# Kernel optimization log

Hardware: AMD Instinct MI355X
Metric: run time of the kernel (lower is better)

## Reference

```python
import jax, jax.numpy as jnp
import numpy as np

B, N, FN, FE, OUT = 64, 128, 64, 16, 128
S, VOCAB, EMB, LH = 1033, 1033, 50, 8
MOMO, SIDE, T = 200, 963, 3
LN_EPS, BN_EPS = 1e-12, 1e-5


def setup_inputs():
    key = jax.random.key(0)
    ks = iter(jax.random.split(key, 64))
    def nrm(shape, scale=0.05):
        return jax.random.normal(next(ks), shape, dtype=jnp.float32) * scale
    inp = {}
    inp['adjacency_1'] = (jax.random.uniform(next(ks), (B, N, N)) < 0.1).astype(jnp.float32)
    inp['nodes_1'] = nrm((B, N, FN), 1.0)
    inp['edges_1'] = nrm((B, N, N, FE), 1.0)
    inp['adjacency_2'] = (jax.random.uniform(next(ks), (B, N, N)) < 0.1).astype(jnp.float32)
    inp['nodes_2'] = nrm((B, N, FN), 1.0)
    inp['edges_2'] = nrm((B, N, N, FE), 1.0)
    inp['d1_momo_fts'] = nrm((B, MOMO), 1.0)
    inp['d2_momo_fts'] = nrm((B, MOMO), 1.0)
    inp['d1_protein_fts'] = jax.random.randint(next(ks), (B, S), 0, VOCAB)
    inp['d2_protein_fts'] = jax.random.randint(next(ks), (B, S), 0, VOCAB)
    inp['side_effect'] = nrm((B, SIDE), 1.0)
    inp['word_emb'] = nrm((VOCAB, EMB))
    inp['pos_emb'] = nrm((VOCAB, EMB))
    inp['ln_gamma'] = jnp.ones((EMB,), jnp.float32)
    inp['ln_beta'] = jnp.zeros((EMB,), jnp.float32)
    inp['W_ih'] = nrm((4 * LH, EMB))
    inp['W_hh'] = nrm((4 * LH, LH))
    inp['b_ih'] = jnp.zeros((4 * LH,), jnp.float32)
    inp['b_hh'] = jnp.zeros((4 * LH,), jnp.float32)
    inp['dec_W1'] = nrm((LH * S, 256))
    inp['dec_b1'] = jnp.zeros((256,), jnp.float32)
    inp['bn_gamma'] = jnp.ones((256,), jnp.float32)
    inp['bn_beta'] = jnp.zeros((256,), jnp.float32)
    inp['dec_W2'] = nrm((256, 45))
    inp['dec_b2'] = jnp.zeros((45,), jnp.float32)
    for g in ('1', '2'):
        inp['W_msg' + g] = nrm((FN, FN))
        inp['W_edge' + g] = nrm((FE, FN))
        inp['W_up' + g] = nrm((2 * FN, FN))
        inp['b_up' + g] = jnp.zeros((FN,), jnp.float32)
        inp['W_read' + g] = nrm((2 * FN, OUT))
        inp['b_read' + g] = jnp.zeros((OUT,), jnp.float32)
    inp['W_momo'] = nrm((MOMO, 45))
    inp['b_momo'] = jnp.zeros((45,), jnp.float32)
    inp['W_side'] = nrm((SIDE, 32))
    inp['b_side'] = jnp.zeros((32,), jnp.float32)
    inp['W_final'] = nrm((2 * (OUT + 45 + 45) + 32, 1))
    inp['b_final'] = jnp.zeros((1,), jnp.float32)
    return inp


def _mpnn(adj, nodes, edges, W_msg, W_edge, W_up, b_up, W_read, b_read):
    # Dense-masked equivalent of the padded neighbor/edge gather construction:
    # message[b,n] = sum_m adj[b,n,m] * (h[b,m] @ W_msg + e[b,n,m] @ W_edge)
    node_mask = adj.sum(-1) > 0  # [B,N] -- only connected nodes are updated
    edge_msg = jnp.einsum('bnm,bnmf,fk->bnk', adj, edges, W_edge)  # static over passes
    h = nodes
    for _ in range(T):
        msg = jnp.einsum('bnm,bmf,fk->bnk', adj, h, W_msg) + edge_msg
        upd = jax.nn.relu(jnp.concatenate([h, msg], -1) @ W_up + b_up)
        h = jnp.where(node_mask[..., None], upd, h)
    r = jax.nn.relu(jnp.concatenate([h, nodes], -1) @ W_read + b_read)  # [B,N,OUT]
    return jnp.einsum('bn,bnk->bk', node_mask.astype(h.dtype), r)


def _protein(ids, word_emb, pos_emb, ln_gamma, ln_beta, W_ih, W_hh, b_ih, b_hh,
             dec_W1, dec_b1, bn_gamma, bn_beta, dec_W2, dec_b2):
    x = word_emb[ids] + pos_emb[jnp.arange(S)][None]  # [B,S,EMB]
    u = x.mean(-1, keepdims=True)
    s = ((x - u) ** 2).mean(-1, keepdims=True)
    x = ln_gamma * (x - u) / jnp.sqrt(s + LN_EPS) + ln_beta
    def step(carry, xt):  # torch LSTM gate order: i, f, g, o
        h, c = carry
        gates = xt @ W_ih.T + b_ih + h @ W_hh.T + b_hh
        i, f, g, o = jnp.split(gates, 4, axis=-1)
        c = jax.nn.sigmoid(f) * c + jax.nn.sigmoid(i) * jnp.tanh(g)
        h = jax.nn.sigmoid(o) * jnp.tanh(c)
        return (h, c), h
    h0 = jnp.zeros((ids.shape[0], LH), jnp.float32)
    _, hs = jax.lax.scan(step, (h0, h0), jnp.swapaxes(x, 0, 1))  # [S,B,LH]
    p = jnp.swapaxes(hs, 0, 1).reshape(ids.shape[0], -1)  # [B, S*LH]
    p = jax.nn.relu(p @ dec_W1 + dec_b1)
    m, v = p.mean(0), p.var(0)  # BatchNorm1d in training mode (batch stats)
    p = bn_gamma * (p - m) / jnp.sqrt(v + BN_EPS) + bn_beta
    return p @ dec_W2 + dec_b2  # [B,45]


def reference(adjacency_1, nodes_1, edges_1, adjacency_2, nodes_2, edges_2,
              d1_momo_fts, d1_protein_fts, d2_momo_fts, d2_protein_fts, side_effect,
              word_emb, pos_emb, ln_gamma, ln_beta, W_ih, W_hh, b_ih, b_hh,
              dec_W1, dec_b1, bn_gamma, bn_beta, dec_W2, dec_b2,
              W_msg1, W_edge1, W_up1, b_up1, W_read1, b_read1,
              W_msg2, W_edge2, W_up2, b_up2, W_read2, b_read2,
              W_momo, b_momo, W_side, b_side, W_final, b_final):
    out1 = _mpnn(adjacency_1, nodes_1, edges_1, W_msg1, W_edge1, W_up1, b_up1, W_read1, b_read1)
    out2 = _mpnn(adjacency_2, nodes_2, edges_2, W_msg2, W_edge2, W_up2, b_up2, W_read2, b_read2)
    p1 = _protein(d1_protein_fts, word_emb, pos_emb, ln_gamma, ln_beta, W_ih, W_hh, b_ih, b_hh,
                  dec_W1, dec_b1, bn_gamma, bn_beta, dec_W2, dec_b2)
    p2 = _protein(d2_protein_fts, word_emb, pos_emb, ln_gamma, ln_beta, W_ih, W_hh, b_ih, b_hh,
                  dec_W1, dec_b1, bn_gamma, bn_beta, dec_W2, dec_b2)
    momo1 = d1_momo_fts @ W_momo + b_momo
    momo2 = d2_momo_fts @ W_momo + b_momo
    drug1 = jnp.concatenate([out1, p1, momo1], axis=1)
    drug2 = jnp.concatenate([out2, p2, momo2], axis=1)
    side = side_effect @ W_side + b_side
    feats = jnp.concatenate([drug1, drug2, side], axis=1)
    return feats @ W_final + b_final  # [B,1]
```

## Files before the change

kernel.cpp:

```cpp
#include <hip/hip_runtime.h>
#include <hip/hip_bf16.h>
#include <math.h>

#define Bb 64
#define Nn 128
#define FNf 64
#define Ss 1033
#define EMBe 50

typedef float f4 __attribute__((ext_vector_type(4)));
typedef float f2 __attribute__((ext_vector_type(2)));
typedef int   i4 __attribute__((ext_vector_type(4)));

#define HS_PSIZE 528896

constexpr size_t OFF_EMSG  = 2*524288 + 2*524288;
constexpr size_t OFF_MASK  = OFF_EMSG  + 2*524288;
constexpr size_t OFF_OUT12 = OFF_MASK  + 2*8192;
constexpr size_t OFF_PPRE  = OFF_OUT12 + 2*8192;
constexpr size_t OFF_PBN   = OFF_PPRE  + 2*16384;
constexpr size_t OFF_XW    = OFF_PBN   + 2*16384;
constexpr size_t OFF_HS    = OFF_XW    + 2*2115584;
constexpr size_t OFF_W2F   = OFF_HS    + 2*HS_PSIZE;
constexpr size_t OFF_WMF   = OFF_W2F   + 2*256;
constexpr size_t OFF_WSF   = OFF_WMF   + 2*200;
constexpr size_t OFF_CONST = OFF_WSF   + 964;
constexpr size_t OFF_COUNT = OFF_CONST + 4;
constexpr size_t OFF_NZ    = OFF_COUNT + 2*8192;
constexpr size_t OFF_AVAL  = OFF_NZ    + 2*524288;

__device__ inline f4 relu4(f4 v) {
  v[0] = fmaxf(v[0], 0.f); v[1] = fmaxf(v[1], 0.f);
  v[2] = fmaxf(v[2], 0.f); v[3] = fmaxf(v[3], 0.f);
  return v;
}

#define ROR16(x, n) __int_as_float(__builtin_amdgcn_update_dpp(0, __float_as_int(x), 0x120 + (n), 0xF, 0xF, true))

__global__ __launch_bounds__(256) void kA(
    const float* __restrict__ adj1, const float* __restrict__ adj2,
    const float* __restrict__ edges1, const float* __restrict__ edges2,
    const float* __restrict__ We1, const float* __restrict__ We2,
    const int* __restrict__ ids1, const int* __restrict__ ids2,
    const float* __restrict__ we, const float* __restrict__ pe,
    const float* __restrict__ lng, const float* __restrict__ lnb,
    const float* __restrict__ Wih, const float* __restrict__ bih,
    const float* __restrict__ bhh, float* __restrict__ ws) {
  int bid = blockIdx.x;
  int t = threadIdx.x;
  if (bid < 4096) {
    int g = bid >> 11;
    int w = t >> 6, lane = t & 63;
    int row = (bid & 2047) * 4 + w;
    const float* adj   = g ? adj2 : adj1;
    const float* edges = g ? edges2 : edges1;
    const float* We    = g ? We2 : We1;
    float* emsg  = ws + OFF_EMSG + (size_t)g * 524288;
    int*   cntg  = (int*)(ws + OFF_COUNT) + (size_t)g * 8192;
    int*   nz    = (int*)(ws + OFF_NZ)    + (size_t)g * 524288;
    float* aval  = ws + OFF_AVAL + (size_t)g * 524288;

    __shared__ int   lidx[4][64];
    __shared__ float lav[4][64];
    __shared__ float les[4][16];

    const float* arow = adj + (size_t)row * 128;
    float a0 = arow[lane], a1 = arow[64 + lane];
    unsigned long long m0 = __ballot(a0 != 0.f);
    unsigned long long m1 = __ballot(a1 != 0.f);
    int c0 = __popcll(m0);
    int cnt = c0 + __popcll(m1);
    unsigned long long below = ((unsigned long long)1 << lane) - 1ull;
    if (a0 != 0.f) { int pos = __popcll(m0 & below); if (pos < 64) { lidx[w][pos] = lane; lav[w][pos] = a0; } }
    if (a1 != 0.f) { int pos = c0 + __popcll(m1 & below); if (pos < 64) { lidx[w][pos] = lane + 64; lav[w][pos] = a1; } }
    int cc = cnt > 64 ? 64 : cnt;
    __syncthreads();

    nz[(size_t)row * 64 + lane]   = (lane < cc) ? lidx[w][lane] : 0;
    aval[(size_t)row * 64 + lane] = (lane < cc) ? lav[w][lane] : 0.f;

    int f = lane & 15, js = lane >> 4;
    float es = 0.f;
    const float* erow = edges + (size_t)row * 128 * 16;
    for (int j = js; j < cc; j += 4) es += lav[w][j] * erow[lidx[w][j] * 16 + f];
    es += __shfl_xor(es, 16);
    es += __shfl_xor(es, 32);
    if (lane < 16) les[w][lane] = es;
    __syncthreads();

    float acc = 0.f;
    #pragma unroll
    for (int ff = 0; ff < 16; ++ff) acc += les[w][ff] * We[ff * 64 + lane];
    emsg[(size_t)row * 64 + lane] = acc;
    if (lane == 0) cntg[row] = cc;
    return;
  }
  int bid6 = bid - 4096;
  int p = bid6 / 2066;
  int xb = bid6 % 2066;
  const int* ids = p ? ids2 : ids1;
  float* xw = ws + OFF_XW + (size_t)p * 2115584;
  __shared__ float wlds[1600];
  __shared__ float glds[50], blds[50], bs[32];
  __shared__ float xl6[8][52];
  for (int i = t; i < 1600; i += 256) wlds[i] = Wih[i];
  if (t < 50) { glds[t] = lng[t]; blds[t] = lnb[t]; }
  if (t < 32) bs[t] = bih[t] + bhh[t];
  __syncthreads();
  int grp = t >> 5, tl = t & 31;
  int newpos = (tl < 16) ? 2 * tl : 2 * tl - 31;
  const float L = 1.44269504088896f;
  float scale = (tl >= 16 && tl < 24) ? -2.f * L : -L;
  int q0 = xb * 32 + grp * 4;
  for (int qq = 0; qq < 4; ++qq) {
    int q = q0 + qq;
    int s = q % Ss;
    int id = ids[q];
    const float* wr = we + (size_t)id * 50;
    const float* pr = pe + (size_t)s * 50;
    float x1 = wr[tl] + pr[tl];
    bool has2 = (tl + 32) < 50;
    float x2 = has2 ? (wr[tl + 32] + pr[tl + 32]) : 0.f;
    float sm = x1 + x2, sq = x1 * x1 + x2 * x2;
    #pragma unroll
    for (int off = 16; off; off >>= 1) {
      sm += __shfl_xor(sm, off, 32);
      sq += __shfl_xor(sq, off, 32);
    }
    float u = sm * (1.f / 50.f);
    float var = fmaxf(sq * (1.f / 50.f) - u * u, 0.f);
    float rstd = rsqrtf(var + 1e-12f);
    xl6[grp][tl] = glds[tl] * (x1 - u) * rstd + blds[tl];
    if (has2) xl6[grp][tl + 32] = glds[tl + 32] * (x2 - u) * rstd + blds[tl + 32];
    __builtin_amdgcn_wave_barrier();
    float acc = bs[tl];
    #pragma unroll 10
    for (int k = 0; k < 50; ++k) acc += xl6[grp][k] * wlds[tl * 50 + k];
    xw[(size_t)q * 32 + newpos] = acc * scale;
    __builtin_amdgcn_wave_barrier();
  }
}

__global__ __launch_bounds__(256) void kB(
    const float* __restrict__ nodes1, const float* __restrict__ nodes2,
    const float* __restrict__ Wm1, const float* __restrict__ Wm2,
    const float* __restrict__ Wup1, const float* __restrict__ Wup2,
    const float* __restrict__ bup1, const float* __restrict__ bup2,
    const float* __restrict__ Wr1, const float* __restrict__ Wr2,
    const float* __restrict__ br1, const float* __restrict__ br2,
    const float* __restrict__ Whh, float* __restrict__ ws) {
  __shared__ __attribute__((aligned(16))) float hl[8192];
  __shared__ __attribute__((aligned(16))) float xl[8192];
  __shared__ __attribute__((aligned(16))) float wml[4096];
  __shared__ __attribute__((aligned(16))) float wbl[8192];
  int bid = blockIdx.x;
  int t = threadIdx.x;
  if (bid >= 128) {
    if (t >= 64) return;
    int idx = bid - 128;
    int p = idx >> 4, xb = idx & 15;
    const float* xw = ws + OFF_XW + (size_t)p * 2115584;
    float* hs = ws + OFF_HS + (size_t)p * HS_PSIZE;
    int lane16 = t & 15;
    int k = lane16 & 7;
    int half = lane16 >> 3;
    int b = xb * 4 + (t >> 4);
    const float* xwp = xw + (size_t)b * (Ss * 32) + lane16 * 2;
    float* hq = hs + (size_t)b * 8 + k;
    const float L = 1.44269504088896f;
    int ga = half ? 8 + k : k;
    int gb = half ? 24 + k : 16 + k;
    float sb_scale = half ? -L : -2.f * L;
    float wa[8], wb[8];
    #pragma unroll
    for (int r = 0; r < 8; ++r) {
      int j = (k - r) & 7;
      wa[r] = -L * Whh[ga * 8 + j];
      wb[r] = sb_scale * Whh[gb * 8 + j];
    }
    float A = half ? 0.f : -4.f * L;
    float B = half ? 1.f : 2.f * L;
    float ho = 0.f, cs = 0.f;

    f2 x[8];
    #pragma unroll
    for (int j = 0; j < 8; ++j) x[j] = *(const f2*)(xwp + (size_t)j * 32);
    const float* pf = xwp + 8 * 32;

    auto step = [&](f2 xc) {
      float h1 = ROR16(ho, 1);
      float h2 = ROR16(ho, 2);
      float h3 = ROR16(ho, 3);
      float h4 = ROR16(ho, 4);
      float h5 = ROR16(ho, 5);
      float h6 = ROR16(ho, 6);
      float h7 = ROR16(ho, 7);
      float a0 = fmaf(ho, wa[0], xc.x);
      float b0 = fmaf(ho, wb[0], xc.y);
      a0 = fmaf(h1, wa[1], a0);  b0 = fmaf(h1, wb[1], b0);
      a0 = fmaf(h2, wa[2], a0);  b0 = fmaf(h2, wb[2], b0);
      a0 = fmaf(h3, wa[3], a0);  b0 = fmaf(h3, wb[3], b0);
      float a1 = h4 * wa[4];     float b1 = h4 * wb[4];
      a1 = fmaf(h5, wa[5], a1);  b1 = fmaf(h5, wb[5], b1);
      a1 = fmaf(h6, wa[6], a1);  b1 = fmaf(h6, wb[6], b1);
      a1 = fmaf(h7, wa[7], a1);  b1 = fmaf(h7, wb[7], b1);
      float acc_a = a0 + a1;
      float acc_b = b0 + b1;
      float ea = __builtin_amdgcn_exp2f(acc_a);
      float sa = __builtin_amdgcn_rcpf(1.f + ea);
      float eb = __builtin_amdgcn_exp2f(acc_b);
      float tb = __builtin_amdgcn_rcpf(1.f + eb);
      float x_own = fmaf(sa * A, tb, sa * B);
      float x_oth = ROR16(x_own, 8);
      float t_oth = ROR16(tb, 8);
      float F  = half ? x_own : x_oth;
      float P2 = half ? x_oth : x_own;
      cs = fmaf(F, cs, P2);
      float e2 = __builtin_amdgcn_exp2f(cs);
      float tc = __builtin_amdgcn_rcpf(1.f + e2);
      float so = half ? tb : t_oth;
      ho = fmaf(so + so, tc, -so);
    };

    for (int g = 0; g < 129; ++g) {
      #pragma unroll
      for (int j = 0; j < 8; ++j) {
        f2 xc = x[j];
        x[j] = *(const f2*)(pf + j * 32);
        step(xc);
        if (!half) *hq = ho;
        hq += 512;
      }
      pf += 256;
    }
    step(x[0]);
    if (!half) *hq = ho;
    return;
  }
  int g = bid >> 6, b = bid & 63;
  const float* nodes = g ? nodes2 : nodes1;
  const float* Wm  = g ? Wm2 : Wm1;
  const float* Wup = g ? Wup2 : Wup1;
  const float* bup = g ? bup2 : bup1;
  const float* Wr  = g ? Wr2 : Wr1;
  const float* br  = g ? br2 : br1;
  const float* emsg = ws + OFF_EMSG + (size_t)g * 524288;
  const int*   cntg = (const int*)(ws + OFF_COUNT) + (size_t)g * 8192;
  const int*   nz   = (const int*)(ws + OFF_NZ) + (size_t)g * 524288;
  const float* aval = ws + OFF_AVAL + (size_t)g * 524288;
  float* out12 = ws + OFF_OUT12 + (size_t)g * 8192;

  int col4 = (t & 15) * 4, rg = t >> 4;
  int r0 = rg * 8;
  for (int i = t; i < 4096; i += 256) wml[i] = Wm[i];
  for (int i = t; i < 8192; i += 256) wbl[i] = Wup[i];
  for (int i = t; i < 8192; i += 256) hl[i] = nodes[(size_t)b * 8192 + i];
  __syncthreads();

  for (int it = 0; it < 3; ++it) {
    {
      f4 acc[8];
      #pragma unroll
      for (int rr = 0; rr < 8; ++rr) acc[rr] = (f4){0.f, 0.f, 0.f, 0.f};
      for (int f0 = 0; f0 < 64; f0 += 4) {
        f4 h4[8];
        #pragma unroll
        for (int rr = 0; rr < 8; ++rr) h4[rr] = *(const f4*)&hl[(r0 + rr) * 64 + f0];
        #pragma unroll
        for (int ff = 0; ff < 4; ++ff) {
          f4 w4 = *(const f4*)&wml[(f0 + ff) * 64 + col4];
          #pragma unroll
          for (int rr = 0; rr < 8; ++rr) acc[rr] += h4[rr][ff] * w4;
        }
      }
      #pragma unroll
      for (int rr = 0; rr < 8; ++rr) *(f4*)&xl[(r0 + rr) * 64 + col4] = acc[rr];
    }
    __syncthreads();
    f4 msgv[8];
    #pragma unroll
    for (int rr = 0; rr < 8; ++rr) {
      int row = b * 128 + r0 + rr;
      f4 m = *(const f4*)&emsg[(size_t)row * 64 + col4];
      int cnt4 = (cntg[row] + 3) >> 2;
      const i4* nzr = (const i4*)(nz + (size_t)row * 64);
      const f4* avr = (const f4*)(aval + (size_t)row * 64);
      for (int j4 = 0; j4 < cnt4; ++j4) {
        i4 nq = nzr[j4];
        f4 aq = avr[j4];
        m += aq[0] * *(const f4*)&xl[nq[0] * 64 + col4];
        m += aq[1] * *(const f4*)&xl[nq[1] * 64 + col4];
        m += aq[2] * *(const f4*)&xl[nq[2] * 64 + col4];
        m += aq[3] * *(const f4*)&xl[nq[3] * 64 + col4];
      }
      msgv[rr] = m;
    }
    __syncthreads();
    #pragma unroll
    for (int rr = 0; rr < 8; ++rr) *(f4*)&xl[(r0 + rr) * 64 + col4] = msgv[rr];
    __syncthreads();
    {
      f4 u[8];
      #pragma unroll
      for (int rr = 0; rr < 8; ++rr) u[rr] = *(const f4*)&bup[col4];
      for (int f0 = 0; f0 < 64; f0 += 4) {
        f4 h4[8];
        #pragma unroll
        for (int rr = 0; rr < 8; ++rr) h4[rr] = *(const f4*)&hl[(r0 + rr) * 64 + f0];
        #pragma unroll
        for (int ff = 0; ff < 4; ++ff) {
          f4 w4 = *(const f4*)&wbl[(f0 + ff) * 64 + col4];
          #pragma unroll
          for (int rr = 0; rr < 8; ++rr) u[rr] += h4[rr][ff] * w4;
        }
      }
      for (int f0 = 0; f0 < 64; f0 += 4) {
        f4 m4[8];
        #pragma unroll
        for (int rr = 0; rr < 8; ++rr) m4[rr] = *(const f4*)&xl[(r0 + rr) * 64 + f0];
        #pragma unroll
        for (int ff = 0; ff < 4; ++ff) {
          f4 w4 = *(const f4*)&wbl[(64 + f0 + ff) * 64 + col4];
          #pragma unroll
          for (int rr = 0; rr < 8; ++rr) u[rr] += m4[rr][ff] * w4;
        }
      }
      __syncthreads();
      #pragma unroll
      for (int rr = 0; rr < 8; ++rr) {
        int row = b * 128 + r0 + rr;
        if (cntg[row] > 0) *(f4*)&hl[(r0 + rr) * 64 + col4] = relu4(u[rr]);
      }
    }
    __syncthreads();
  }

  for (int i = t; i < 8192; i += 256) xl[i] = nodes[(size_t)b * 8192 + i];
  __syncthreads();
  for (int kt = 0; kt < 2; ++kt) {
    for (int i = t; i < 8192; i += 256) {
      int f = i >> 6, c = i & 63;
      wbl[i] = Wr[f * 128 + kt * 64 + c];
    }
    __syncthreads();
    f4 part = {0.f, 0.f, 0.f, 0.f};
    {
      f4 u[8];
      #pragma unroll
      for (int rr = 0; rr < 8; ++rr) u[rr] = *(const f4*)&br[kt * 64 + col4];
      for (int f0 = 0; f0 < 64; f0 += 4) {
        f4 h4[8];
        #pragma unroll
        for (int rr = 0; rr < 8; ++rr) h4[rr] = *(const f4*)&hl[(r0 + rr) * 64 + f0];
        #pragma unroll
        for (int ff = 0; ff < 4; ++ff) {
          f4 w4 = *(const f4*)&wbl[(f0 + ff) * 64 + col4];
          #pragma unroll
          for (int rr = 0; rr < 8; ++rr) u[rr] += h4[rr][ff] * w4;
        }
      }
      for (int f0 = 0; f0 < 64; f0 += 4) {
        f4 n4[8];
        #pragma unroll
        for (int rr = 0; rr < 8; ++rr) n4[rr] = *(const f4*)&xl[(r0 + rr) * 64 + f0];
        #pragma unroll
        for (int ff = 0; ff < 4; ++ff) {
          f4 w4 = *(const f4*)&wbl[(64 + f0 + ff) * 64 + col4];
          #pragma unroll
          for (int rr = 0; rr < 8; ++rr) u[rr] += n4[rr][ff] * w4;
        }
      }
      #pragma unroll
      for (int rr = 0; rr < 8; ++rr) {
        int row = b * 128 + r0 + rr;
        if (cntg[row] > 0) part += relu4(u[rr]);
      }
    }
    *(f4*)&wml[rg * 64 + col4] = part;
    __syncthreads();
    for (int off = 8; off; off >>= 1) {
      if (rg < off) {
        f4 v = *(f4*)&wml[rg * 64 + col4] + *(f4*)&wml[(rg + off) * 64 + col4];
        *(f4*)&wml[rg * 64 + col4] = v;
      }
      __syncthreads();
    }
    if (rg == 0) *(f4*)&out12[(size_t)b * 128 + kt * 64 + col4] = *(f4*)&wml[col4];
    __syncthreads();
  }
}

__global__ __launch_bounds__(256) void kC(
    const float* __restrict__ W1,
    const float* __restrict__ W2, const float* __restrict__ b2,
    const float* __restrict__ Wm, const float* __restrict__ bm,
    const float* __restrict__ Wsd, const float* __restrict__ bsd,
    const float* __restrict__ Wf, const float* __restrict__ bf,
    float* __restrict__ ws) {
  int bid = blockIdx.x;
  int t = threadIdx.x;
  if (bid < 256) {
    int ks = bid & 31, jt = (bid >> 5) & 3, p = bid >> 7;
    const float* hs = ws + OFF_HS + (size_t)p * HS_PSIZE;
    float* pp = ws + OFF_PPRE + (size_t)p * 16384;
    int s0 = ks * 33;
    int s1 = s0 + 33; if (s1 > Ss) s1 = Ss;
    int j0 = jt * 64;
    __shared__ __attribute__((aligned(16))) float hsl[3][64 * 12];
    __shared__ __attribute__((aligned(16))) float w1l[3][512];
    int jl = (t & 15) * 4, bb = t >> 4;
    f4 acc[4] = {};
    int wb = (2 * t) & 7;
    int wbrow = t >> 2;
    for (int sb = s0; sb < s1; sb += 3) {
      int ns = s1 - sb; if (ns > 3) ns = 3;
      for (int ss = 0; ss < ns; ++ss) {
        int s = sb + ss;
        f2 v = *(const f2*)&hs[(size_t)s * 512 + 2 * t];
        *(f2*)&hsl[ss][wbrow * 12 + wb] = v;
        if (t < 128) {
          *(f4*)&w1l[ss][(t >> 4) * 64 + (t & 15) * 4] =
              *(const f4*)&W1[(size_t)(s * 8 + (t >> 4)) * 256 + j0 + (t & 15) * 4];
        }
      }
      __syncthreads();
      for (int ss = 0; ss < 3; ++ss) {
        if (ss >= ns) break;
        f4 r[4][2];
        #pragma unroll
        for (int i = 0; i < 4; ++i) {
          int b = bb + 16 * i;
          r[i][0] = *(const f4*)&hsl[ss][b * 12];
          r[i][1] = *(const f4*)&hsl[ss][b * 12 + 4];
        }
        #pragma unroll
        for (int l = 0; l < 8; ++l) {
          f4 wv = *(const f4*)&w1l[ss][l * 64 + jl];
          #pragma unroll
          for (int i = 0; i < 4; ++i) {
            float hv = (l < 4) ? r[i][0][l] : r[i][1][l - 4];
            acc[i] += hv * wv;
          }
        }
      }
      __syncthreads();
    }
    #pragma unroll
    for (int i = 0; i < 4; ++i) {
      int b = bb + 16 * i;
      float* dst = pp + (size_t)b * 256 + j0 + jl;
      atomicAdd(dst + 0, acc[i][0]); atomicAdd(dst + 1, acc[i][1]);
      atomicAdd(dst + 2, acc[i][2]); atomicAdd(dst + 3, acc[i][3]);
    }
    return;
  }
  __shared__ float wf[468];
  for (int i = t; i < 468; i += 256) wf[i] = Wf[i];
  __syncthreads();
  float* w2f = ws + OFF_W2F;
  float* wmf = ws + OFF_WMF;
  float* wsf = ws + OFF_WSF;
  float* cst = ws + OFF_CONST;
  {
    float a1 = 0.f, a2 = 0.f;
    for (int k = 0; k < 45; ++k) {
      float v = W2[t * 45 + k];
      a1 += v * wf[128 + k];
      a2 += v * wf[346 + k];
    }
    w2f[t] = a1; w2f[256 + t] = a2;
  }
  if (t < 200) {
    float a1 = 0.f, a2 = 0.f;
    for (int k = 0; k < 45; ++k) {
      float v = Wm[t * 45 + k];
      a1 += v * wf[173 + k];
      a2 += v * wf[391 + k];
    }
    wmf[t] = a1; wmf[200 + t] = a2;
  }
  for (int i = t; i < 963; i += 256) {
    float a = 0.f;
    for (int k = 0; k < 32; ++k) a += Wsd[i * 32 + k] * wf[436 + k];
    wsf[i] = a;
  }
  if (t == 0) {
    float cc = bf[0];
    for (int k = 0; k < 45; ++k)
      cc += b2[k] * (wf[128 + k] + wf[346 + k]) + bm[k] * (wf[173 + k] + wf[391 + k]);
    for (int k = 0; k < 32; ++k) cc += bsd[k] * wf[436 + k];
    cst[0] = cc;
  }
}

__global__ __launch_bounds__(256) void kD(
    const float* __restrict__ b1, const float* __restrict__ bng,
    const float* __restrict__ bnb,
    const float* __restrict__ d1m, const float* __restrict__ d2m,
    const float* __restrict__ se, const float* __restrict__ Wf,
    float* __restrict__ ws, float* __restrict__ out) {
  int b = blockIdx.x, t = threadIdx.x;
  const float* out12 = ws + OFF_OUT12;
  const float* pp0 = ws + OFF_PPRE;
  const float* pp1 = ws + OFF_PPRE + 16384;
  const float* w2f = ws + OFF_W2F;
  const float* wmf = ws + OFF_WMF;
  const float* wsf = ws + OFF_WSF;
  float bj = b1[t];
  float sm0 = 0.f, sq0 = 0.f, sm1 = 0.f, sq1 = 0.f;
  for (int bb = 0; bb < 64; ++bb) {
    float v0 = fmaxf(pp0[bb * 256 + t] + bj, 0.f);
    float v1 = fmaxf(pp1[bb * 256 + t] + bj, 0.f);
    sm0 += v0; sq0 += v0 * v0;
    sm1 += v1; sq1 += v1 * v1;
  }
  float m0 = sm0 * (1.f / 64.f);
  float var0 = fmaxf(sq0 * (1.f / 64.f) - m0 * m0, 0.f);
  float rstd0 = rsqrtf(var0 + 1e-5f);
  float sc0 = bng[t] * rstd0, sh0 = bnb[t] - m0 * sc0;
  float m1 = sm1 * (1.f / 64.f);
  float var1 = fmaxf(sq1 * (1.f / 64.f) - m1 * m1, 0.f);
  float rstd1 = rsqrtf(var1 + 1e-5f);
  float sc1 = bng[t] * rstd1, sh1 = bnb[t] - m1 * sc1;
  float val0 = sc0 * fmaxf(pp0[b * 256 + t] + bj, 0.f) + sh0;
  float val1 = sc1 * fmaxf(pp1[b * 256 + t] + bj, 0.f) + sh1;
  float acc = val0 * w2f[t] + val1 * w2f[256 + t];
  if (t < 128) {
    acc += out12[b * 128 + t] * Wf[t];
    acc += out12[8192 + b * 128 + t] * Wf[218 + t];
  }
  if (t < 200) {
    acc += d1m[b * 200 + t] * wmf[t];
    acc += d2m[b * 200 + t] * wmf[200 + t];
  }
  for (int i = t; i < 963; i += 256) acc += se[b * 963 + i] * wsf[i];
  __shared__ float red[256];
  red[t] = acc;
  __syncthreads();
  for (int off = 128; off; off >>= 1) {
    if (t < off) red[t] += red[t + off];
    __syncthreads();
  }
  if (t == 0) out[b] = red[0] + (ws + OFF_CONST)[0];
}

extern "C" void kernel_launch(void* const* d_in, const int* in_sizes, int n_in,
                              void* d_out, int out_size, void* d_ws, size_t ws_size,
                              hipStream_t stream) {
  const float* adj1  = (const float*)d_in[0];
  const float* nodes1= (const float*)d_in[1];
  const float* edges1= (const float*)d_in[2];
  const float* adj2  = (const float*)d_in[3];
  const float* nodes2= (const float*)d_in[4];
  const float* edges2= (const float*)d_in[5];
  const float* d1m   = (const float*)d_in[6];
  const float* d2m   = (const float*)d_in[7];
  const int*   ids1  = (const int*)d_in[8];
  const int*   ids2  = (const int*)d_in[9];
  const float* se    = (const float*)d_in[10];
  const float* we    = (const float*)d_in[11];
  const float* pe    = (const float*)d_in[12];
  const float* lng   = (const float*)d_in[13];
  const float* lnb   = (const float*)d_in[14];
  const float* Wih   = (const float*)d_in[15];
  const float* Whh   = (const float*)d_in[16];
  const float* bih   = (const float*)d_in[17];
  const float* bhh   = (const float*)d_in[18];
  const float* W1    = (const float*)d_in[19];
  const float* b1    = (const float*)d_in[20];
  const float* bng   = (const float*)d_in[21];
  const float* bnb   = (const float*)d_in[22];
  const float* W2    = (const float*)d_in[23];
  const float* b2    = (const float*)d_in[24];
  const float* Wm1   = (const float*)d_in[25];
  const float* We1   = (const float*)d_in[26];
  const float* Wup1  = (const float*)d_in[27];
  const float* bup1  = (const float*)d_in[28];
  const float* Wr1   = (const float*)d_in[29];
  const float* br1   = (const float*)d_in[30];
  const float* Wm2   = (const float*)d_in[31];
  const float* We2   = (const float*)d_in[32];
  const float* Wup2  = (const float*)d_in[33];
  const float* bup2  = (const float*)d_in[34];
  const float* Wr2   = (const float*)d_in[35];
  const float* br2   = (const float*)d_in[36];
  const float* Wmo   = (const float*)d_in[37];
  const float* bmo   = (const float*)d_in[38];
  const float* Wsd   = (const float*)d_in[39];
  const float* bsd   = (const float*)d_in[40];
  const float* Wf    = (const float*)d_in[41];
  const float* bf    = (const float*)d_in[42];
  float* ws = (float*)d_ws;
  float* out = (float*)d_out;

  hipMemsetAsync(ws + OFF_PPRE, 0, 2 * 16384 * sizeof(float), stream);

  kA<<<8228, 256, 0, stream>>>(adj1, adj2, edges1, edges2, We1, We2,
                               ids1, ids2, we, pe, lng, lnb, Wih, bih, bhh, ws);
  kB<<<160, 256, 0, stream>>>(nodes1, nodes2, Wm1, Wm2, Wup1, Wup2, bup1, bup2,
                              Wr1, Wr2, br1, br2, Whh, ws);
  kC<<<257, 256, 0, stream>>>(W1, W2, b2, Wmo, bmo, Wsd, bsd, Wf, bf, ws);
  kD<<<64, 256, 0, stream>>>(b1, bng, bnb, d1m, d2m, se, Wf, ws, out);
}
```

Measured before the change: 249.2 us.

## Store LSTM hidden states time-contiguous and load them as vec4 in decoder GEMM

Result: faster. 226.8 us (-9.0%).

```diff
diff --git a/kernel.cpp b/kernel.cpp
--- a/kernel.cpp
+++ b/kernel.cpp
@@ -12,7 +12,9 @@
 typedef float f2 __attribute__((ext_vector_type(2)));
 typedef int   i4 __attribute__((ext_vector_type(4)));
 
-#define HS_PSIZE 528896
+#define HS_KSTRIDE 1036
+#define HS_BSTRIDE 8288
+#define HS_PSIZE   530432
 
 constexpr size_t OFF_EMSG  = 2*524288 + 2*524288;
 constexpr size_t OFF_MASK  = OFF_EMSG  + 2*524288;
@@ -166,7 +168,7 @@
     int half = lane16 >> 3;
     int b = xb * 4 + (t >> 4);
     const float* xwp = xw + (size_t)b * (Ss * 32) + lane16 * 2;
-    float* hq = hs + (size_t)b * 8 + k;
+    float* hq = hs + (size_t)b * HS_BSTRIDE + (size_t)k * HS_KSTRIDE;
     const float L = 1.44269504088896f;
     int ga = half ? 8 + k : k;
     int gb = half ? 24 + k : 16 + k;
@@ -181,6 +183,7 @@
     float A = half ? 0.f : -4.f * L;
     float B = half ? 1.f : 2.f * L;
     float ho = 0.f, cs = 0.f;
+    float q0v = 0.f, q1v = 0.f, q2v = 0.f, q3v = 0.f;
 
     f2 x[8];
     #pragma unroll
@@ -228,13 +231,17 @@
         f2 xc = x[j];
         x[j] = *(const f2*)(pf + j * 32);
         step(xc);
-        if (!half) *hq = ho;
-        hq += 512;
+        if (j == 0 || j == 4) q0v = ho;
+        else if (j == 1 || j == 5) q1v = ho;
+        else if (j == 2 || j == 6) q2v = ho;
+        else if (j == 3) { q3v = ho; if (!half) *(f4*)(hq + 0) = (f4){q0v, q1v, q2v, q3v}; }
+        else { q3v = ho; if (!half) *(f4*)(hq + 4) = (f4){q0v, q1v, q2v, q3v}; }
       }
       pf += 256;
+      hq += 8;
     }
     step(x[0]);
-    if (!half) *hq = ho;
+    if (!half) hq[0] = ho;
     return;
   }
   int g = bid >> 6, b = bid & 63;
@@ -403,29 +410,34 @@
     int ks = bid & 31, jt = (bid >> 5) & 3, p = bid >> 7;
     const float* hs = ws + OFF_HS + (size_t)p * HS_PSIZE;
     float* pp = ws + OFF_PPRE + (size_t)p * 16384;
-    int s0 = ks * 33;
-    int s1 = s0 + 33; if (s1 > Ss) s1 = Ss;
+    int s0 = ks * 32;
+    int s1 = (ks == 31) ? Ss : s0 + 32;
     int j0 = jt * 64;
-    __shared__ __attribute__((aligned(16))) float hsl[3][64 * 12];
-    __shared__ __attribute__((aligned(16))) float w1l[3][512];
+    __shared__ __attribute__((aligned(16))) float hsl[4][768];
+    __shared__ __attribute__((aligned(16))) float w1l[4][512];
     int jl = (t & 15) * 4, bb = t >> 4;
     f4 acc[4] = {};
-    int wb = (2 * t) & 7;
-    int wbrow = t >> 2;
-    for (int sb = s0; sb < s1; sb += 3) {
-      int ns = s1 - sb; if (ns > 3) ns = 3;
-      for (int ss = 0; ss < ns; ++ss) {
+    for (int sb = s0; sb < s1; sb += 4) {
+      #pragma unroll
+      for (int u = 0; u < 2; ++u) {
+        int bk = t + 256 * u;
+        int b = bk >> 3, k = bk & 7;
+        f4 v = *(const f4*)&hs[(size_t)b * HS_BSTRIDE + (size_t)k * HS_KSTRIDE + sb];
+        int c = b * 12 + k;
+        hsl[0][c] = v[0]; hsl[1][c] = v[1]; hsl[2][c] = v[2]; hsl[3][c] = v[3];
+      }
+      #pragma unroll
+      for (int u = 0; u < 2; ++u) {
+        int idx = t + 256 * u;
+        int ss = idx >> 7, l = (idx >> 4) & 7, jj = (idx & 15) * 4;
         int s = sb + ss;
-        f2 v = *(const f2*)&hs[(size_t)s * 512 + 2 * t];
-        *(f2*)&hsl[ss][wbrow * 12 + wb] = v;
-        if (t < 128) {
-          *(f4*)&w1l[ss][(t >> 4) * 64 + (t & 15) * 4] =
-              *(const f4*)&W1[(size_t)(s * 8 + (t >> 4)) * 256 + j0 + (t & 15) * 4];
-        }
+        f4 wv = (s < Ss) ? *(const f4*)&W1[(size_t)(s * 8 + l) * 256 + j0 + jj]
+                         : (f4){0.f, 0.f, 0.f, 0.f};
+        *(f4*)&w1l[ss][l * 64 + jj] = wv;
       }
       __syncthreads();
-      for (int ss = 0; ss < 3; ++ss) {
-        if (ss >= ns) break;
+      #pragma unroll
+      for (int ss = 0; ss < 4; ++ss) {
         f4 r[4][2];
         #pragma unroll
         for (int i = 0; i < 4; ++i) {
```
